# Optimization experiments

Hardware: AMD Instinct MI355X
Metric: run time of the kernel (lower is better)

## Reference

```python
import jax, jax.numpy as jnp
import numpy as np

B, S, H, A = 64, 4096, 256, 128


def entmax15(z):
    # exact entmax-1.5 along the last axis (Peters & Martins 2019)
    z = z / 2.0
    z = z - jnp.max(z, axis=-1, keepdims=True)
    zs = -jnp.sort(-z, axis=-1)                      # descending sort
    n = zs.shape[-1]
    k = jnp.arange(1, n + 1, dtype=z.dtype)
    mean = jnp.cumsum(zs, axis=-1) / k
    mean_sq = jnp.cumsum(zs * zs, axis=-1) / k
    ss = k * (mean_sq - mean * mean)
    delta = jnp.clip((1.0 - ss) / k, 0.0)
    tau = mean - jnp.sqrt(delta)
    k_star = jnp.sum(tau <= zs, axis=-1)             # support size per row
    tau_star = jnp.take_along_axis(tau, (k_star - 1)[..., None], axis=-1)
    return jnp.square(jnp.clip(z - tau_star, 0.0))


def setup_inputs() -> dict:
    key = jax.random.key(0)
    k0, k1, k2, k3, k4 = jax.random.split(key, 5)
    lim1 = 1.0 / np.sqrt(H)
    lim2 = 1.0 / np.sqrt(A)
    return {
        "lstm_output": jax.random.normal(k0, (B, S, H), dtype=jnp.float32),
        "W1": jax.random.uniform(k1, (H, A), jnp.float32, -lim1, lim1),
        "b1": jax.random.uniform(k2, (A,), jnp.float32, -lim1, lim1),
        "W2": jax.random.uniform(k3, (A, 1), jnp.float32, -lim2, lim2),
        "b2": jax.random.uniform(k4, (1,), jnp.float32, -lim2, lim2),
    }


def reference(lstm_output, W1, b1, W2, b2):
    # score MLP: Linear -> Tanh -> Linear -> squeeze(-1)  => [B, S]
    h = jnp.tanh(jnp.einsum("bsh,ha->bsa", lstm_output, W1) + b1)
    scores = (jnp.einsum("bsa,ao->bso", h, W2) + b2)[..., 0]
    weights = entmax15(scores)                       # entmax over seq axis (dim=1)
    context = jnp.einsum("bsh,bs->bh", lstm_output, weights)
    return (context, weights)
```

## Files before the change

### kernel.cpp

```cpp
#include <hip/hip_runtime.h>
#include <hip/hip_bf16.h>

#define BB 64
#define SS 4096
#define HH 256
#define AA 128

typedef _Float16 half8v __attribute__((ext_vector_type(8)));
typedef float floatx16 __attribute__((ext_vector_type(16)));

__device__ __forceinline__ float fast_tanh(float x) {
    float xc = fminf(fmaxf(x, -9.0f), 9.0f);
    float e = __expf(2.0f * xc);
    return 1.0f - __fdividef(2.0f, e + 1.0f);
}

__global__ void convert_w1(const float* __restrict__ W1, _Float16* __restrict__ Wt) {
    int n = blockIdx.x;
    int k = threadIdx.x;
    Wt[n * HH + k] = (_Float16)W1[k * AA + n];
}

__global__ __launch_bounds__(256, 2) void score_ldsb(
    const float* __restrict__ X,
    const _Float16* __restrict__ Wt,
    const float* __restrict__ b1,
    const float* __restrict__ W2,
    const float* __restrict__ b2,
    float* __restrict__ scores)
{
    __shared__ _Float16 Bs[32768];

    const int tid   = threadIdx.x;
    const int wid   = tid >> 6;
    const int lane  = tid & 63;
    const int lrow  = lane & 31;
    const int lhalf = lane >> 5;

    #pragma unroll
    for (int i = 0; i < 16; ++i) {
        int f = tid + i * 256;
        int n = f & 127, kh = f >> 7;
        *(uint4*)(Bs + (size_t)f * 8) = *(const uint4*)(Wt + (size_t)n * HH + kh * 8);
    }
    __syncthreads();

    float cb1[4], cw2[4];
    #pragma unroll
    for (int nt = 0; nt < 4; ++nt) {
        cb1[nt] = b1[nt * 32 + lrow];
        cw2[nt] = W2[nt * 32 + lrow];
    }
    const float bias2 = b2[0];

    const int gw = blockIdx.x * 4 + wid;

    #pragma unroll 1
    for (int t = 0; t < 4; ++t) {
        const int m0 = (gw * 4 + t) * 32;
        const float* xp = X + (size_t)(m0 + lrow) * HH + lhalf * 8;

        floatx16 acc[4];
        #pragma unroll
        for (int nt = 0; nt < 4; ++nt)
            #pragma unroll
            for (int r = 0; r < 16; ++r) acc[nt][r] = 0.0f;

        #pragma unroll
        for (int k2 = 0; k2 < 16; ++k2) {
            float4 v0 = *(const float4*)(xp + k2 * 16);
            float4 v1 = *(const float4*)(xp + k2 * 16 + 4);
            half8v a;
            a[0] = (_Float16)v0.x; a[1] = (_Float16)v0.y;
            a[2] = (_Float16)v0.z; a[3] = (_Float16)v0.w;
            a[4] = (_Float16)v1.x; a[5] = (_Float16)v1.y;
            a[6] = (_Float16)v1.z; a[7] = (_Float16)v1.w;
            const _Float16* bp = Bs + ((size_t)(k2 * 2 + lhalf) * 128 + lrow) * 8;
            #pragma unroll
            for (int nt = 0; nt < 4; ++nt) {
                half8v b = *(const half8v*)(bp + nt * 32 * 8);
                acc[nt] = __builtin_amdgcn_mfma_f32_32x32x16_f16(a, b, acc[nt], 0, 0, 0);
            }
        }

        #pragma unroll
        for (int r = 0; r < 16; ++r) {
            float v = 0.0f;
            #pragma unroll
            for (int nt = 0; nt < 4; ++nt)
                v += fast_tanh(acc[nt][r] + cb1[nt]) * cw2[nt];
            #pragma unroll
            for (int o = 1; o < 32; o <<= 1) v += __shfl_xor(v, o);
            if (lrow == 0)
                scores[m0 + (r & 3) + 8 * (r >> 2) + 4 * lhalf] = v + bias2;
        }
    }
}

__global__ __launch_bounds__(256) void entmax_kernel(
    float* __restrict__ buf, float* __restrict__ ctx)
{
    __shared__ float sred[4];
    const int b = blockIdx.x, tid = threadIdx.x;
    float* p = buf + (size_t)b * SS;

    float z[16];
    #pragma unroll
    for (int j = 0; j < 16; ++j) z[j] = p[tid + j * 256] * 0.5f;

    float m = -1e30f;
    #pragma unroll
    for (int j = 0; j < 16; ++j) m = fmaxf(m, z[j]);
    #pragma unroll
    for (int o = 1; o < 64; o <<= 1) m = fmaxf(m, __shfl_xor(m, o));
    if ((tid & 63) == 0) sred[tid >> 6] = m;
    __syncthreads();
    m = fmaxf(fmaxf(sred[0], sred[1]), fmaxf(sred[2], sred[3]));
    __syncthreads();
    #pragma unroll
    for (int j = 0; j < 16; ++j) z[j] -= m;

    float lo = -1.0f, hi = 0.0f;
    for (int it = 0; it < 35; ++it) {
        float tau = 0.5f * (lo + hi);
        float s = 0.0f;
        #pragma unroll
        for (int j = 0; j < 16; ++j) {
            float d = fmaxf(z[j] - tau, 0.0f);
            s = fmaf(d, d, s);
        }
        #pragma unroll
        for (int o = 1; o < 64; o <<= 1) s += __shfl_xor(s, o);
        if ((tid & 63) == 0) sred[tid >> 6] = s;
        __syncthreads();
        s = sred[0] + sred[1] + sred[2] + sred[3];
        __syncthreads();
        if (s >= 1.0f) lo = tau; else hi = tau;
    }
    const float tau = 0.5f * (lo + hi);

    #pragma unroll
    for (int j = 0; j < 16; ++j) {
        float d = fmaxf(z[j] - tau, 0.0f);
        p[tid + j * 256] = d * d;
    }
    ctx[b * HH + tid] = 0.0f;
}

__global__ __launch_bounds__(256) void context_kernel(
    const float* __restrict__ X, const float* __restrict__ w,
    float* __restrict__ ctx)
{
    const int b  = blockIdx.y;
    const int s0 = blockIdx.x * 128;
    const int h  = threadIdx.x;

    __shared__ float ws_[128];
    __shared__ int nzflag;
    if (h == 0) nzflag = 0;
    __syncthreads();
    if (h < 128) {
        float v = w[(size_t)b * SS + s0 + h];
        ws_[h] = v;
        if (v > 0.0f) nzflag = 1;
    }
    __syncthreads();
    if (!nzflag) return;

    float acc = 0.0f;
    const float* xp = X + ((size_t)b * SS + s0) * HH + h;
    #pragma unroll 4
    for (int i = 0; i < 128; ++i) {
        float wv = ws_[i];
        if (wv != 0.0f) acc = fmaf(xp[(size_t)i * HH], wv, acc);
    }
    atomicAdd(&ctx[b * HH + h], acc);
}

extern "C" void kernel_launch(void* const* d_in, const int* in_sizes, int n_in,
                              void* d_out, int out_size, void* d_ws, size_t ws_size,
                              hipStream_t stream) {
    const float* X  = (const float*)d_in[0];
    const float* W1 = (const float*)d_in[1];
    const float* b1 = (const float*)d_in[2];
    const float* W2 = (const float*)d_in[3];
    const float* b2 = (const float*)d_in[4];

    float* out = (float*)d_out;
    float* ctx = out;
    float* wts = out + BB * HH;
    _Float16* Wt = (_Float16*)d_ws;

    convert_w1<<<AA, HH, 0, stream>>>(W1, Wt);
    score_ldsb<<<512, 256, 0, stream>>>(X, Wt, b1, W2, b2, wts);
    entmax_kernel<<<BB, 256, 0, stream>>>(wts, ctx);
    context_kernel<<<dim3(SS / 128, BB), 256, 0, stream>>>(X, wts, ctx);
}
```

Measured before the change: 442.0 us.

## Restructure score GEMM with async global-to-LDS double-buffered K-chunks

Replaces the per-wave direct-global-load score kernel with a 128-row tiled kernel that streams X and W1 in K-chunks of 32 through double-buffered LDS, using global_load_lds async copies and XOR-swizzled layouts. Waves split the work 2x2 over rows and output columns, and partial score sums are reduced through LDS. The aim is to overlap memory traffic with MFMA work and raise occupancy, since W1 is no longer fully resident in 64KB of LDS. The cost is a barrier per chunk, W1 reloaded by every block, and many more blocks (2048 instead of 512).

```diff
diff --git a/kernel.cpp b/kernel.cpp
--- a/kernel.cpp
+++ b/kernel.cpp
@@ -5,6 +5,9 @@
 #define SS 4096
 #define HH 256
 #define AA 128
+#define MT 128
+#define BK 32
+#define NCHUNK (HH / BK)
 
 typedef _Float16 half8v __attribute__((ext_vector_type(8)));
 typedef float floatx16 __attribute__((ext_vector_type(16)));
@@ -15,13 +18,19 @@
     return 1.0f - __fdividef(2.0f, e + 1.0f);
 }
 
+__device__ __forceinline__ void async16(const void* g, void* l) {
+    __builtin_amdgcn_global_load_lds(
+        (const __attribute__((address_space(1))) unsigned int*)g,
+        (__attribute__((address_space(3))) unsigned int*)l, 16, 0, 0);
+}
+
 __global__ void convert_w1(const float* __restrict__ W1, _Float16* __restrict__ Wt) {
     int n = blockIdx.x;
     int k = threadIdx.x;
     Wt[n * HH + k] = (_Float16)W1[k * AA + n];
 }
 
-__global__ __launch_bounds__(256, 2) void score_ldsb(
+__global__ __launch_bounds__(256, 3) void score_dma(
     const float* __restrict__ X,
     const _Float16* __restrict__ Wt,
     const float* __restrict__ b1,
@@ -29,72 +38,110 @@
     const float* __restrict__ b2,
     float* __restrict__ scores)
 {
-    __shared__ _Float16 Bs[32768];
+    __shared__ float    Xs[2][4096];
+    __shared__ _Float16 Bsh[2][4096];
+    __shared__ float    red[2][128];
 
     const int tid   = threadIdx.x;
     const int wid   = tid >> 6;
     const int lane  = tid & 63;
     const int lrow  = lane & 31;
     const int lhalf = lane >> 5;
-
-    #pragma unroll
-    for (int i = 0; i < 16; ++i) {
-        int f = tid + i * 256;
-        int n = f & 127, kh = f >> 7;
-        *(uint4*)(Bs + (size_t)f * 8) = *(const uint4*)(Wt + (size_t)n * HH + kh * 8);
-    }
-    __syncthreads();
-
-    float cb1[4], cw2[4];
-    #pragma unroll
-    for (int nt = 0; nt < 4; ++nt) {
-        cb1[nt] = b1[nt * 32 + lrow];
-        cw2[nt] = W2[nt * 32 + lrow];
-    }
-    const float bias2 = b2[0];
-
-    const int gw = blockIdx.x * 4 + wid;
+    const int rh    = wid >> 1;
+    const int ch    = wid & 1;
+    const int m0    = blockIdx.x * MT;
+
+    const int xr = tid >> 3;
+    const int xg = (tid & 7) ^ (xr & 7);
+    const float* xgp = X + (size_t)(m0 + xr) * HH + xg * 4;
+    const int bn = tid >> 2;
+    const int bg = (tid & 3) ^ (bn & 3);
+    const _Float16* bgp = Wt + (size_t)bn * HH + bg * 8;
+
+    float cb1[2], cw2[2];
+    #pragma unroll
+    for (int ct = 0; ct < 2; ++ct) {
+        int col = ch * 64 + ct * 32 + lrow;
+        cb1[ct] = b1[col];
+        cw2[ct] = W2[col];
+    }
+
+    floatx16 acc[2][2];
+    #pragma unroll
+    for (int rt = 0; rt < 2; ++rt)
+        #pragma unroll
+        for (int ct = 0; ct < 2; ++ct)
+            #pragma unroll
+            for (int r = 0; r < 16; ++r) acc[rt][ct][r] = 0.0f;
+
+    #pragma unroll
+    for (int i = 0; i < 4; ++i)
+        async16(xgp + (size_t)i * 32 * HH, (char*)&Xs[0][0] + i * 4096 + wid * 1024);
+    #pragma unroll
+    for (int i = 0; i < 2; ++i)
+        async16(bgp + (size_t)i * 64 * HH, (char*)&Bsh[0][0] + i * 4096 + wid * 1024);
+    __syncthreads();
 
     #pragma unroll 1
-    for (int t = 0; t < 4; ++t) {
-        const int m0 = (gw * 4 + t) * 32;
-        const float* xp = X + (size_t)(m0 + lrow) * HH + lhalf * 8;
-
-        floatx16 acc[4];
-        #pragma unroll
-        for (int nt = 0; nt < 4; ++nt)
-            #pragma unroll
-            for (int r = 0; r < 16; ++r) acc[nt][r] = 0.0f;
-
-        #pragma unroll
-        for (int k2 = 0; k2 < 16; ++k2) {
-            float4 v0 = *(const float4*)(xp + k2 * 16);
-            float4 v1 = *(const float4*)(xp + k2 * 16 + 4);
-            half8v a;
-            a[0] = (_Float16)v0.x; a[1] = (_Float16)v0.y;
-            a[2] = (_Float16)v0.z; a[3] = (_Float16)v0.w;
-            a[4] = (_Float16)v1.x; a[5] = (_Float16)v1.y;
-            a[6] = (_Float16)v1.z; a[7] = (_Float16)v1.w;
-            const _Float16* bp = Bs + ((size_t)(k2 * 2 + lhalf) * 128 + lrow) * 8;
-            #pragma unroll
-            for (int nt = 0; nt < 4; ++nt) {
-                half8v b = *(const half8v*)(bp + nt * 32 * 8);
-                acc[nt] = __builtin_amdgcn_mfma_f32_32x32x16_f16(a, b, acc[nt], 0, 0, 0);
+    for (int c = 0; c < NCHUNK; ++c) {
+        if (c + 1 < NCHUNK) {
+            const int k0 = (c + 1) * BK;
+            const int nb = (c + 1) & 1;
+            #pragma unroll
+            for (int i = 0; i < 4; ++i)
+                async16(xgp + (size_t)i * 32 * HH + k0,
+                        (char*)&Xs[nb][0] + i * 4096 + wid * 1024);
+            #pragma unroll
+            for (int i = 0; i < 2; ++i)
+                async16(bgp + (size_t)i * 64 * HH + k0,
+                        (char*)&Bsh[nb][0] + i * 4096 + wid * 1024);
+        }
+        const float*    xb = &Xs[c & 1][0];
+        const _Float16* bb = &Bsh[c & 1][0];
+        #pragma unroll
+        for (int s = 0; s < 2; ++s) {
+            half8v bf[2];
+            #pragma unroll
+            for (int ct = 0; ct < 2; ++ct) {
+                int n = ch * 64 + ct * 32 + lrow;
+                int idx = n * 4 + ((s * 2 + lhalf) ^ (n & 3));
+                bf[ct] = *(const half8v*)(bb + (size_t)idx * 8);
             }
-        }
-
+            #pragma unroll
+            for (int rt = 0; rt < 2; ++rt) {
+                int r  = rh * 64 + rt * 32 + lrow;
+                int g0 = s * 4 + lhalf * 2;
+                int i0 = r * 8 + (g0 ^ (r & 7));
+                int i1 = r * 8 + ((g0 + 1) ^ (r & 7));
+                float4 va = *(const float4*)(xb + (size_t)i0 * 4);
+                float4 vb = *(const float4*)(xb + (size_t)i1 * 4);
+                half8v a;
+                a[0] = (_Float16)va.x; a[1] = (_Float16)va.y;
+                a[2] = (_Float16)va.z; a[3] = (_Float16)va.w;
+                a[4] = (_Float16)vb.x; a[5] = (_Float16)vb.y;
+                a[6] = (_Float16)vb.z; a[7] = (_Float16)vb.w;
+                acc[rt][0] = __builtin_amdgcn_mfma_f32_32x32x16_f16(a, bf[0], acc[rt][0], 0, 0, 0);
+                acc[rt][1] = __builtin_amdgcn_mfma_f32_32x32x16_f16(a, bf[1], acc[rt][1], 0, 0, 0);
+            }
+        }
+        if (c + 1 < NCHUNK) __syncthreads();
+    }
+
+    #pragma unroll
+    for (int rt = 0; rt < 2; ++rt) {
         #pragma unroll
         for (int r = 0; r < 16; ++r) {
-            float v = 0.0f;
-            #pragma unroll
-            for (int nt = 0; nt < 4; ++nt)
-                v += fast_tanh(acc[nt][r] + cb1[nt]) * cw2[nt];
+            float v = fast_tanh(acc[rt][0][r] + cb1[0]) * cw2[0]
+                    + fast_tanh(acc[rt][1][r] + cb1[1]) * cw2[1];
             #pragma unroll
             for (int o = 1; o < 32; o <<= 1) v += __shfl_xor(v, o);
             if (lrow == 0)
-                scores[m0 + (r & 3) + 8 * (r >> 2) + 4 * lhalf] = v + bias2;
-        }
-    }
+                red[ch][rh * 64 + rt * 32 + (r & 3) + 8 * (r >> 2) + 4 * lhalf] = v;
+        }
+    }
+    __syncthreads();
+    if (tid < MT)
+        scores[m0 + tid] = b2[0] + red[0][tid] + red[1][tid];
 }
 
 __global__ __launch_bounds__(256) void entmax_kernel(
@@ -192,7 +239,7 @@
     _Float16* Wt = (_Float16*)d_ws;
 
     convert_w1<<<AA, HH, 0, stream>>>(W1, Wt);
-    score_ldsb<<<512, 256, 0, stream>>>(X, Wt, b1, W2, b2, wts);
+    score_dma<<<(BB * SS) / MT, 256, 0, stream>>>(X, Wt, b1, W2, b2, wts);
     entmax_kernel<<<BB, 256, 0, stream>>>(wts, ctx);
     context_kernel<<<dim3(SS / 128, BB), 256, 0, stream>>>(X, wts, ctx);
 }
```

After: 406.6 us. -8.0%, faster.
